# Kernel tuning notes

Hardware: AMD Instinct MI355X
Metric: run time of the kernel (lower is better)

The kernel has to match this reference:

```python
import jax, jax.numpy as jnp
import numpy as np

B, S, N = 8, 4, 64
ATOM_FDIM, BOND_FDIM, H = 133, 147, 300
DEPTH = 3


def setup_inputs() -> dict:
    key = jax.random.key(0)
    ks = jax.random.split(key, 9)
    f_atoms = jax.random.normal(ks[0], (B, S, N, ATOM_FDIM), dtype=jnp.float32)
    f_bonds = jax.random.uniform(ks[1], (B, S, N, N, BOND_FDIM), dtype=jnp.float32)
    adj = (jax.random.uniform(ks[2], (B, S, N, N)) < 0.3).astype(jnp.float32)
    def lin(k, fan_in, fan_out):
        return jax.random.normal(k, (fan_in, fan_out), dtype=jnp.float32) / np.sqrt(fan_in)
    return {
        'f_atoms': f_atoms,
        'f_bonds': f_bonds,
        'adj': adj,
        'W_i_atom': lin(ks[3], ATOM_FDIM, H),   # bias=False
        'W_i_bond': lin(ks[4], BOND_FDIM, H),   # bias=False
        'W_h_0': lin(ks[5], H, H),              # bias=False
        'W_h_1': lin(ks[6], H, H),              # bias=False
        'W_o': lin(ks[7], 3 * H, H),            # bias=True
        'b_o': jax.random.normal(ks[8], (H,), dtype=jnp.float32) * 0.01,
    }


def reference(f_atoms, f_bonds, adj, W_i_atom, W_i_bond, W_h_0, W_h_1, W_o, b_o):
    act = jax.nn.relu
    # atom / bond input embeddings
    input_atom = act(f_atoms @ W_i_atom)                        # [B,S,N,H]
    message_atom = input_atom
    input_bond = act((adj[..., None] * f_bonds) @ W_i_bond)     # [B,S,N,N,H]
    message_bond = input_bond
    for W_h in (W_h_0, W_h_1):  # depth-1 message-passing steps
        agg = message_bond.sum(axis=2) * jax.nn.sigmoid(message_bond.max(axis=2))  # [B,S,N,H]
        message_atom = message_atom + agg
        resonance = jnp.einsum('bsnd,bsmd->bsnm', message_atom, message_atom) * adj  # [B,S,N,N]
        # broadcast atom messages along edges, subtract reverse message
        mb = adj[..., None] * message_atom[:, :, None, :, :] - message_bond  # [B,S,N,N,H]
        mb = jnp.swapaxes(mb, 2, 3)  # permute(0,1,3,2,4)
        mb = act(input_bond + mb @ W_h)
        message_bond = mb * jax.nn.softmax(resonance, axis=2)[..., None]
    agg = message_bond.sum(axis=2) * jax.nn.sigmoid(message_bond.max(axis=2))
    a_input = jnp.concatenate([agg, message_atom, input_atom], axis=-1)  # [B,S,N,3H]
    atom_hiddens = act(a_input @ W_o + b_o)  # [B,S,N,H]
    return atom_hiddens, message_bond
```

## Files before the change

### kernel.cpp

```cpp
#include <hip/hip_runtime.h>
#include <hip/hip_bf16.h>
#include <math.h>

#define Bc 8
#define Sc 4
#define Nc 64
#define AF 133
#define BFD 147
#define Hc 300
#define BS (Bc*Sc)
#define ROWS (BS*Nc)
#define EDGES (BS*Nc*Nc)
#define BSLICE 19456
#define BHALF  9728

typedef float f32x4 __attribute__((ext_vector_type(4)));
typedef short bf16x8 __attribute__((ext_vector_type(8)));
union U4 { uint4 u; bf16x8 v; };

__device__ __forceinline__ float reluf(float x){ return fmaxf(x, 0.f); }
__device__ __forceinline__ float b2f(unsigned short u){ union{unsigned int i;float f;}v; v.i = ((unsigned int)u)<<16; return v.f; }
__device__ __forceinline__ unsigned short f2b(float f){ __hip_bfloat16 h = __float2bfloat16(f); return *reinterpret_cast<unsigned short*>(&h); }
__device__ __forceinline__ void split2(float x, unsigned short &hi, unsigned short &lo){
    unsigned short h = f2b(x);
    float r = x - b2f(h);
    hi = h; lo = f2b(r);
}

__global__ __launch_bounds__(320) void k_atom_embed(const float* __restrict__ f_atoms,
        const float* __restrict__ W, float* __restrict__ input_atom, float* __restrict__ message_atom){
    __shared__ float x[AF];
    int row = blockIdx.x;
    const float* fr = f_atoms + (size_t)row*AF;
    for (int d = threadIdx.x; d < AF; d += blockDim.x) x[d] = fr[d];
    __syncthreads();
    int h = threadIdx.x;
    if (h < Hc){
        float acc = 0.f;
        for (int d = 0; d < AF; ++d) acc = fmaf(x[d], W[d*Hc + h], acc);
        float v = reluf(acc);
        input_atom[(size_t)row*Hc + h] = v;
        message_atom[(size_t)row*Hc + h] = v;
    }
}

__global__ __launch_bounds__(256) void k_prep_wp2(const float* __restrict__ W, int K, int NKT,
        unsigned short* __restrict__ WP){
    int idx = blockIdx.x*256 + threadIdx.x;
    if (idx >= NKT*BSLICE) return;
    int j  = idx & 7;
    int l  = (idx >> 3) & 63;
    int ct = (idx >> 9) % 19;
    int rem = idx / BHALF;
    int hl = rem & 1;
    int kt = rem >> 1;
    int col = ct*16 + (l & 15);
    int k   = kt*32 + (l >> 4)*8 + j;
    float v = (col < Hc && k < K) ? W[k*Hc + col] : 0.f;
    unsigned short hi, lo; split2(v, hi, lo);
    WP[idx] = hl ? lo : hi;
}

template<int MODE>
__global__ __launch_bounds__(1024) void k_gemm_t(
        const float* __restrict__ Asrc,
        const unsigned short* __restrict__ WP,
        const float* __restrict__ ma,
        const float* __restrict__ adj,
        const float* __restrict__ sm,
        const float* __restrict__ ib,
        float* __restrict__ dst)
{
    constexpr int NKT  = MODE ? 10 : 5;
    constexpr int ASTR = MODE ? 300 : BFD;

    __shared__ unsigned short sAhi[4096];
    __shared__ unsigned short sAlo[4096];
    __shared__ unsigned short sB[BSLICE];
    __shared__ int s_eOut[128];
    __shared__ int s_eRev[128];
    __shared__ float s_adjRev[128];
    __shared__ int s_aAtom[128];

    const int t = threadIdx.x;
    if (MODE){
        if (t < 128){
            int r = t;
            int bs = blockIdx.x >> 5, kk = blockIdx.x & 31;
            int s1 = 64-kk, s2 = 127-2*kk, s3 = 128-kk;
            int a, b;
            if (r < s1){ a = kk; b = kk + r; }
            else if (r < s2){ a = kk+1 + (r - s1); b = kk; }
            else if (r < s3){ a = 63-kk; b = 63-kk + (r - s2); }
            else { a = 64-kk + (r - s3); b = 63-kk; }
            int eo = (bs*64 + a)*64 + b;
            int er = (bs*64 + b)*64 + a;
            s_eOut[r] = eo; s_eRev[r] = er; s_aAtom[r] = bs*64 + a;
            s_adjRev[r] = adj[er];
        }
        __syncthreads();
    }

    const int rt_b = t >> 7;
    const int q_b  = (t >> 5) & 3;
    const int li_b = (t >> 1) & 15;
    const int half = t & 1;
    const int brow = rt_b*16 + li_b;
    const int koff = q_b*8 + 4*half;
    const float* aRow;
    const float* mRow = nullptr;
    float adjR = 0.f;
    if (MODE){
        aRow = Asrc + (size_t)s_eRev[brow]*ASTR;
        mRow = ma + (size_t)s_aAtom[brow]*Hc;
        adjR = s_adjRev[brow];
    } else {
        int e = blockIdx.x*128 + brow;
        aRow = Asrc + (size_t)e*ASTR;
        adjR = adj[e];
    }

    float pm[4], pa[4];
    auto prefetchA = [&](int kt){
        int k0 = kt*32 + koff;
        if (MODE){
            if (k0 <= 296){
                float4 v = *(const float4*)(aRow + k0);
                float4 w = *(const float4*)(mRow + k0);
                pm[0]=v.x; pm[1]=v.y; pm[2]=v.z; pm[3]=v.w;
                pa[0]=w.x; pa[1]=w.y; pa[2]=w.z; pa[3]=w.w;
            }
        } else {
            #pragma unroll
            for (int j = 0; j < 4; ++j){
                int k = k0 + j;
                pm[j] = (k < BFD) ? aRow[k] : 0.f;
            }
        }
    };
    auto buildA = [&](int kt){
        int k0 = kt*32 + koff;
        float xv[4];
        if (MODE){
            if (k0 <= 296){
                #pragma unroll
                for (int j = 0; j < 4; ++j) xv[j] = fmaf(adjR, pa[j], -pm[j]);
            } else { xv[0]=xv[1]=xv[2]=xv[3]=0.f; }
        } else {
            #pragma unroll
            for (int j = 0; j < 4; ++j) xv[j] = adjR * pm[j];
        }
        unsigned short h0,l0,h1,l1,h2,l2,h3,l3;
        split2(xv[0],h0,l0); split2(xv[1],h1,l1);
        split2(xv[2],h2,l2); split2(xv[3],h3,l3);
        uint2 hw, lw;
        hw.x = (unsigned int)h0 | ((unsigned int)h1<<16);
        hw.y = (unsigned int)h2 | ((unsigned int)h3<<16);
        lw.x = (unsigned int)l0 | ((unsigned int)l1<<16);
        lw.y = (unsigned int)l2 | ((unsigned int)l3<<16);
        *(uint2*)&sAhi[4*t] = hw;
        *(uint2*)&sAlo[4*t] = lw;
    };
    auto copyB = [&](int kt){
        const unsigned short* src = WP + (size_t)kt*BSLICE;
        #pragma unroll
        for (int rep = 0; rep < 3; ++rep){
            int i = t + rep*1024;
            if (i < BSLICE/8){
                uint4 v = *(const uint4*)(src + i*8);
                *(uint4*)&sB[i*8] = v;
            }
        }
    };

    const int wv = t >> 6, lane = t & 63;
    const int li = lane & 15, quad = lane >> 4;
    const int rg = wv & 3;
    const int cg = wv >> 2;
    const int c0 = cg*5;
    const int myC = (cg < 3) ? 5 : 4;

    f32x4 acc[5][2];
    #pragma unroll
    for (int c = 0; c < 5; ++c){ acc[c][0] = (f32x4){0,0,0,0}; acc[c][1] = (f32x4){0,0,0,0}; }

    prefetchA(0);
    for (int kt = 0; kt < NKT; ++kt){
        if (kt) __syncthreads();
        copyB(kt);
        buildA(kt);
        __syncthreads();
        if (kt+1 < NKT) prefetchA(kt+1);
        U4 a0h, a0l, a1h, a1l;
        a0h.u = *(const uint4*)&sAhi[((2*rg  )*64 + lane)*8];
        a0l.u = *(const uint4*)&sAlo[((2*rg  )*64 + lane)*8];
        a1h.u = *(const uint4*)&sAhi[((2*rg+1)*64 + lane)*8];
        a1l.u = *(const uint4*)&sAlo[((2*rg+1)*64 + lane)*8];
        #pragma unroll
        for (int c = 0; c < 5; ++c){
            if (c < myC){
                U4 bh, bl;
                bh.u = *(const uint4*)&sB[        (c0+c)*512 + lane*8];
                bl.u = *(const uint4*)&sB[BHALF + (c0+c)*512 + lane*8];
                acc[c][0] = __builtin_amdgcn_mfma_f32_16x16x32_bf16(a0h.v, bl.v, acc[c][0], 0,0,0);
                acc[c][0] = __builtin_amdgcn_mfma_f32_16x16x32_bf16(a0l.v, bh.v, acc[c][0], 0,0,0);
                acc[c][0] = __builtin_amdgcn_mfma_f32_16x16x32_bf16(a0h.v, bh.v, acc[c][0], 0,0,0);
                acc[c][1] = __builtin_amdgcn_mfma_f32_16x16x32_bf16(a1h.v, bl.v, acc[c][1], 0,0,0);
                acc[c][1] = __builtin_amdgcn_mfma_f32_16x16x32_bf16(a1l.v, bh.v, acc[c][1], 0,0,0);
                acc[c][1] = __builtin_amdgcn_mfma_f32_16x16x32_bf16(a1h.v, bh.v, acc[c][1], 0,0,0);
            }
        }
    }

    int eO[2][4]; float smv[2][4];
    #pragma unroll
    for (int r2 = 0; r2 < 2; ++r2)
        #pragma unroll
        for (int i = 0; i < 4; ++i){
            int row = (2*rg + r2)*16 + quad*4 + i;
            int e = MODE ? s_eOut[row] : blockIdx.x*128 + row;
            eO[r2][i] = e;
            if (MODE) smv[r2][i] = sm[e];
        }
    #pragma unroll
    for (int c = 0; c < 5; ++c){
        if (c >= myC) continue;
        int h = (c0 + c)*16 + li;
        if (h >= Hc) continue;
        #pragma unroll
        for (int r2 = 0; r2 < 2; ++r2)
            #pragma unroll
            for (int i = 0; i < 4; ++i){
                size_t off = (size_t)eO[r2][i]*Hc + h;
                float v = acc[c][r2][i];
                if (MODE) v = reluf(v + ib[off]) * smv[r2][i];
                else      v = reluf(v);
                dst[off] = v;
            }
    }
}

__global__ __launch_bounds__(320) void k_agg(const float* __restrict__ message_bond,
        float* __restrict__ message_atom, float* __restrict__ agg_out, int final_mode){
    int row = blockIdx.x;
    int bs = row >> 6, m = row & 63;
    int h = threadIdx.x;
    if (h >= Hc) return;
    size_t base = ((size_t)(bs*Nc)*Nc + m)*(size_t)Hc + h;
    float s = 0.f, mx = -INFINITY;
    for (int n = 0; n < Nc; ++n){
        float v = message_bond[base + (size_t)n*Nc*Hc];
        s += v; mx = fmaxf(mx, v);
    }
    float agg = s * (1.f/(1.f + expf(-mx)));
    if (final_mode) agg_out[(size_t)row*Hc + h] = agg;
    else message_atom[(size_t)row*Hc + h] += agg;
}

__global__ __launch_bounds__(256) void k_resonance_softmax(const float* __restrict__ message_atom,
        const float* __restrict__ adj, float* __restrict__ sm){
    int bs = blockIdx.x >> 6, m = blockIdx.x & 63;
    __shared__ float am[Hc];
    __shared__ float res[Nc];
    for (int d = threadIdx.x; d < Hc; d += blockDim.x)
        am[d] = message_atom[((size_t)(bs*Nc)+m)*Hc + d];
    __syncthreads();
    int wave = threadIdx.x >> 6, lane = threadIdx.x & 63;
    for (int n = wave; n < Nc; n += 4){
        const float* man = message_atom + ((size_t)(bs*Nc)+n)*Hc;
        float acc = 0.f;
        for (int d = lane; d < Hc; d += 64) acc = fmaf(man[d], am[d], acc);
        #pragma unroll
        for (int off = 32; off > 0; off >>= 1) acc += __shfl_xor(acc, off, 64);
        if (lane == 0) res[n] = acc * adj[((size_t)(bs*Nc)+n)*Nc + m];
    }
    __syncthreads();
    if (threadIdx.x < Nc){
        float v = res[threadIdx.x];
        float mx = v;
        #pragma unroll
        for (int off = 32; off > 0; off >>= 1) mx = fmaxf(mx, __shfl_xor(mx, off, 64));
        float e = expf(v - mx);
        float ssum = e;
        #pragma unroll
        for (int off = 32; off > 0; off >>= 1) ssum += __shfl_xor(ssum, off, 64);
        sm[((size_t)(bs*Nc)+threadIdx.x)*Nc + m] = e / ssum;
    }
}

#define R7 4
__global__ __launch_bounds__(320) void k_output(const float* __restrict__ agg,
        const float* __restrict__ message_atom, const float* __restrict__ input_atom,
        const float* __restrict__ W_o, const float* __restrict__ b_o, float* __restrict__ out){
    __shared__ float xin[R7][3*Hc];
    int r0 = blockIdx.x * R7;
    for (int idx = threadIdx.x; idx < R7*3*Hc; idx += blockDim.x){
        int r = idx / (3*Hc), k = idx - r*(3*Hc);
        int row = r0 + r;
        float v;
        if (k < Hc)           v = agg[(size_t)row*Hc + k];
        else if (k < 2*Hc)    v = message_atom[(size_t)row*Hc + (k - Hc)];
        else                  v = input_atom[(size_t)row*Hc + (k - 2*Hc)];
        xin[r][k] = v;
    }
    __syncthreads();
    int h = threadIdx.x;
    if (h < Hc){
        float acc[R7];
        #pragma unroll
        for (int r=0;r<R7;r++) acc[r] = b_o[h];
        for (int d = 0; d < 3*Hc; ++d){
            float w = W_o[d*Hc + h];
            #pragma unroll
            for (int r=0;r<R7;r++) acc[r] = fmaf(xin[r][d], w, acc[r]);
        }
        #pragma unroll
        for (int r=0;r<R7;r++) out[(size_t)(r0+r)*Hc + h] = reluf(acc[r]);
    }
}

extern "C" void kernel_launch(void* const* d_in, const int* in_sizes, int n_in,
                              void* d_out, int out_size, void* d_ws, size_t ws_size,
                              hipStream_t stream){
    const float* f_atoms  = (const float*)d_in[0];
    const float* f_bonds  = (const float*)d_in[1];
    const float* adj      = (const float*)d_in[2];
    const float* W_i_atom = (const float*)d_in[3];
    const float* W_i_bond = (const float*)d_in[4];
    const float* W_h0     = (const float*)d_in[5];
    const float* W_h1     = (const float*)d_in[6];
    const float* W_o      = (const float*)d_in[7];
    const float* b_o      = (const float*)d_in[8];

    float* out = (float*)d_out;
    float* atom_hiddens = out;
    float* mb_out = out + (size_t)ROWS*Hc;

    float* wsf = (float*)d_ws;
    float* input_atom   = wsf; wsf += (size_t)ROWS*Hc;
    float* message_atom = wsf; wsf += (size_t)ROWS*Hc;
    float* sm           = wsf; wsf += (size_t)EDGES;
    float* ib           = wsf; wsf += (size_t)EDGES*Hc;
    unsigned short* wsu = (unsigned short*)wsf;
    unsigned short* WP0 = wsu; wsu += 10*BSLICE;
    unsigned short* WP1 = wsu; wsu += 10*BSLICE;
    unsigned short* WPb = wsu; wsu += 5*BSLICE;
    float* agg_out = ib;

    k_atom_embed<<<ROWS, 320, 0, stream>>>(f_atoms, W_i_atom, input_atom, message_atom);
    k_prep_wp2<<<(10*BSLICE + 255)/256, 256, 0, stream>>>(W_h0, Hc, 10, WP0);
    k_prep_wp2<<<(10*BSLICE + 255)/256, 256, 0, stream>>>(W_h1, Hc, 10, WP1);
    k_prep_wp2<<<(5*BSLICE + 255)/256, 256, 0, stream>>>(W_i_bond, BFD, 5, WPb);
    k_gemm_t<0><<<EDGES/128, 1024, 0, stream>>>(f_bonds, WPb, nullptr, adj, nullptr, nullptr, ib);
    k_agg<<<ROWS, 320, 0, stream>>>(ib, message_atom, nullptr, 0);
    k_resonance_softmax<<<ROWS, 256, 0, stream>>>(message_atom, adj, sm);
    k_gemm_t<1><<<BS*32, 1024, 0, stream>>>(ib, WP0, message_atom, adj, sm, ib, mb_out);
    k_agg<<<ROWS, 320, 0, stream>>>(mb_out, message_atom, nullptr, 0);
    k_resonance_softmax<<<ROWS, 256, 0, stream>>>(message_atom, adj, sm);
    k_gemm_t<1><<<BS*32, 1024, 0, stream>>>(mb_out, WP1, message_atom, adj, sm, ib, mb_out);
    k_agg<<<ROWS, 320, 0, stream>>>(mb_out, nullptr, agg_out, 1);
    k_output<<<ROWS/R7, 320, 0, stream>>>(agg_out, message_atom, input_atom, W_o, b_o, atom_hiddens);
}
```

Measured before the change: 821.3 us.

## Use direct global-to-LDS loads, raise MFMA priority, vectorize aggregation kernel

The weight-slice copy in the GEMM now uses global_load_lds to move data straight into shared memory without a round trip through registers. The MFMA section is wrapped in s_setprio so those waves are favoured while other waves prefetch. The aggregation kernel is rewritten so each thread handles four hidden channels with float4 loads, and four rows are processed per block. These changes target register pressure, load instruction count, and memory efficiency in the aggregation passes, which are bandwidth-bound.

```diff
diff --git a/kernel.cpp b/kernel.cpp
--- a/kernel.cpp
+++ b/kernel.cpp
@@ -25,6 +25,12 @@
     unsigned short h = f2b(x);
     float r = x - b2f(h);
     hi = h; lo = f2b(r);
+}
+
+typedef __attribute__((address_space(1))) const unsigned int* gas1_t;
+typedef __attribute__((address_space(3))) unsigned int* las3_t;
+__device__ __forceinline__ void gload_lds16(const void* g, void* l){
+    __builtin_amdgcn_global_load_lds((gas1_t)g, (las3_t)l, 16, 0, 0);
 }
 
 __global__ __launch_bounds__(320) void k_atom_embed(const float* __restrict__ f_atoms,
@@ -166,10 +172,8 @@
         #pragma unroll
         for (int rep = 0; rep < 3; ++rep){
             int i = t + rep*1024;
-            if (i < BSLICE/8){
-                uint4 v = *(const uint4*)(src + i*8);
-                *(uint4*)&sB[i*8] = v;
-            }
+            if (i < BSLICE/8)
+                gload_lds16(src + (size_t)i*8, &sB[i*8]);
         }
     };
 
@@ -191,6 +195,7 @@
         buildA(kt);
         __syncthreads();
         if (kt+1 < NKT) prefetchA(kt+1);
+        __builtin_amdgcn_s_setprio(1);
         U4 a0h, a0l, a1h, a1l;
         a0h.u = *(const uint4*)&sAhi[((2*rg  )*64 + lane)*8];
         a0l.u = *(const uint4*)&sAlo[((2*rg  )*64 + lane)*8];
@@ -210,6 +215,7 @@
                 acc[c][1] = __builtin_amdgcn_mfma_f32_16x16x32_bf16(a1h.v, bh.v, acc[c][1], 0,0,0);
             }
         }
+        __builtin_amdgcn_s_setprio(0);
     }
 
     int eO[2][4]; float smv[2][4];
@@ -242,19 +248,34 @@
 
 __global__ __launch_bounds__(320) void k_agg(const float* __restrict__ message_bond,
         float* __restrict__ message_atom, float* __restrict__ agg_out, int final_mode){
-    int row = blockIdx.x;
+    int t = threadIdx.x;
+    int r = t / 80, c = t - r*80;
+    if (c >= 75) return;
+    int row = blockIdx.x*4 + r;
     int bs = row >> 6, m = row & 63;
-    int h = threadIdx.x;
-    if (h >= Hc) return;
-    size_t base = ((size_t)(bs*Nc)*Nc + m)*(size_t)Hc + h;
-    float s = 0.f, mx = -INFINITY;
+    size_t base = ((size_t)(bs*Nc)*Nc + m)*(size_t)Hc + (size_t)c*4;
+    float4 s  = {0.f, 0.f, 0.f, 0.f};
+    float4 mx = {-INFINITY, -INFINITY, -INFINITY, -INFINITY};
+    #pragma unroll 4
     for (int n = 0; n < Nc; ++n){
-        float v = message_bond[base + (size_t)n*Nc*Hc];
-        s += v; mx = fmaxf(mx, v);
-    }
-    float agg = s * (1.f/(1.f + expf(-mx)));
-    if (final_mode) agg_out[(size_t)row*Hc + h] = agg;
-    else message_atom[(size_t)row*Hc + h] += agg;
+        float4 v = *(const float4*)(message_bond + base + (size_t)n*Nc*Hc);
+        s.x += v.x; s.y += v.y; s.z += v.z; s.w += v.w;
+        mx.x = fmaxf(mx.x, v.x); mx.y = fmaxf(mx.y, v.y);
+        mx.z = fmaxf(mx.z, v.z); mx.w = fmaxf(mx.w, v.w);
+    }
+    float4 agg;
+    agg.x = s.x * (1.f/(1.f + expf(-mx.x)));
+    agg.y = s.y * (1.f/(1.f + expf(-mx.y)));
+    agg.z = s.z * (1.f/(1.f + expf(-mx.z)));
+    agg.w = s.w * (1.f/(1.f + expf(-mx.w)));
+    size_t o = (size_t)row*Hc + (size_t)c*4;
+    if (final_mode){
+        *(float4*)(agg_out + o) = agg;
+    } else {
+        float4 cur = *(const float4*)(message_atom + o);
+        cur.x += agg.x; cur.y += agg.y; cur.z += agg.z; cur.w += agg.w;
+        *(float4*)(message_atom + o) = cur;
+    }
 }
 
 __global__ __launch_bounds__(256) void k_resonance_softmax(const float* __restrict__ message_atom,
@@ -352,12 +373,12 @@
     k_prep_wp2<<<(10*BSLICE + 255)/256, 256, 0, stream>>>(W_h1, Hc, 10, WP1);
     k_prep_wp2<<<(5*BSLICE + 255)/256, 256, 0, stream>>>(W_i_bond, BFD, 5, WPb);
     k_gemm_t<0><<<EDGES/128, 1024, 0, stream>>>(f_bonds, WPb, nullptr, adj, nullptr, nullptr, ib);
-    k_agg<<<ROWS, 320, 0, stream>>>(ib, message_atom, nullptr, 0);
+    k_agg<<<ROWS/4, 320, 0, stream>>>(ib, message_atom, nullptr, 0);
     k_resonance_softmax<<<ROWS, 256, 0, stream>>>(message_atom, adj, sm);
     k_gemm_t<1><<<BS*32, 1024, 0, stream>>>(ib, WP0, message_atom, adj, sm, ib, mb_out);
-    k_agg<<<ROWS, 320, 0, stream>>>(mb_out, message_atom, nullptr, 0);
+    k_agg<<<ROWS/4, 320, 0, stream>>>(mb_out, message_atom, nullptr, 0);
     k_resonance_softmax<<<ROWS, 256, 0, stream>>>(message_atom, adj, sm);
     k_gemm_t<1><<<BS*32, 1024, 0, stream>>>(mb_out, WP1, message_atom, adj, sm, ib, mb_out);
-    k_agg<<<ROWS, 320, 0, stream>>>(mb_out, nullptr, agg_out, 1);
+    k_agg<<<ROWS/4, 320, 0, stream>>>(mb_out, nullptr, agg_out, 1);
     k_output<<<ROWS/R7, 320, 0, stream>>>(agg_out, message_atom, input_atom, W_o, b_o, atom_hiddens);
 }
```

Result: faster. 798.5 us (-2.8%).
